# Kernel tuning notes

Hardware: AMD Instinct MI355X
Metric: run time of the kernel (lower is better)

## Reference

```python
import jax, jax.numpy as jnp
import numpy as np

WINDOW = 11
SIGMA = 1.5
CHANNELS = 3
C1 = 0.01 ** 2
C2 = 0.03 ** 2


def _gaussian_kernel(size=WINDOW, sigma=SIGMA, channels=CHANNELS):
    coords = jnp.arange(size, dtype=jnp.float32) - size // 2
    g = jnp.exp(-coords ** 2 / (2.0 * sigma ** 2))
    g = jnp.outer(g, g)
    g = g / g.sum()
    # depthwise kernel: [C, 1, K, K] (OIHW with feature_group_count=C)
    return jnp.broadcast_to(g[None, None], (channels, 1, size, size))


def _dwconv(x, kernel):
    # x: [N, C, H, W]; SAME padding, depthwise (groups = C)
    pad = WINDOW // 2
    return jax.lax.conv_general_dilated(
        x, kernel,
        window_strides=(1, 1),
        padding=[(pad, pad), (pad, pad)],
        dimension_numbers=('NCHW', 'OIHW', 'NCHW'),
        feature_group_count=CHANNELS,
    )


def setup_inputs() -> dict:
    key = jax.random.key(0)
    k1, k2 = jax.random.split(key)
    shape = (16, 3, 512, 512)
    pred = jax.random.uniform(k1, shape, dtype=jnp.float32)
    target = jax.random.uniform(k2, shape, dtype=jnp.float32)
    return {"pred": pred, "target": target}


def reference(pred, target):
    kernel = _gaussian_kernel().astype(pred.dtype)
    mu_p = _dwconv(pred, kernel)
    mu_t = _dwconv(target, kernel)
    mu_p2 = mu_p * mu_p
    mu_t2 = mu_t * mu_t
    mu_pt = mu_p * mu_t
    sigma_p2 = _dwconv(pred * pred, kernel) - mu_p2
    sigma_t2 = _dwconv(target * target, kernel) - mu_t2
    sigma_pt = _dwconv(pred * target, kernel) - mu_pt
    ssim_map = ((2.0 * mu_pt + C1) * (2.0 * sigma_pt + C2)) / (
        (mu_p2 + mu_t2 + C1) * (sigma_p2 + sigma_t2 + C2)
    )
    return 1.0 - ssim_map.mean()
```

## Files before the change

### kernel.cpp

```cpp
#include <hip/hip_runtime.h>
#include <math.h>

#define IMG_H 512
#define IMG_W 512
#define TILE  32
#define NSLOT 64
#define HT_S  52

typedef _Float16 f16x4 __attribute__((ext_vector_type(4)));
typedef _Float16 f16x8 __attribute__((ext_vector_type(8)));
typedef _Float16 h2    __attribute__((ext_vector_type(2)));
typedef float    f32x4 __attribute__((ext_vector_type(4)));

union F16Frag { f16x8 v8; f16x4 v4[2]; };

__global__ __launch_bounds__(256, 8)
void ssim_main(const float* __restrict__ pred, const float* __restrict__ targ,
               float* __restrict__ partial, double* __restrict__ acc, int mode)
{
    __shared__ _Float16 hT[5][TILE][HT_S];

    const int tid  = threadIdx.x;
    const int lane = tid & 63;
    const int wave = tid >> 6;
    const int ln   = lane & 15;
    const int lg   = lane >> 4;

    const int tx = blockIdx.x, ty = blockIdx.y, img = blockIdx.z;
    const float* __restrict__ p = pred + (size_t)img * (IMG_H * IMG_W);
    const float* __restrict__ t = targ + (size_t)img * (IMG_H * IMG_W);
    const int gr0 = ty * TILE - 5;
    const int wo  = tx * TILE - 8;

    if (tid < 160) {
        int q = tid / 32, col = tid & 31;
        *(h2*)&hT[q][col][42] = h2{(_Float16)0.f, (_Float16)0.f};
        *(h2*)&hT[q][col][44] = h2{(_Float16)0.f, (_Float16)0.f};
        *(h2*)&hT[q][col][46] = h2{(_Float16)0.f, (_Float16)0.f};
    }

    f16x8 Bw, A2w;
    #pragma unroll
    for (int j = 0; j < 8; ++j) {
        int k  = lg * 8 + j;
        int ih = k - ln - 3;
        int iv = k - ln;
        float dh = (float)(ih - 5), dv = (float)(iv - 5);
        float vh = 0.26601173f * exp2f(-dh * dh * 0.32059889f);
        float vv = 0.26601173f * exp2f(-dv * dv * 0.32059889f);
        Bw[j]  = (_Float16)(((unsigned)ih <= 10u) ? vh : 0.0f);
        A2w[j] = (_Float16)(((unsigned)iv <= 10u) ? vv : 0.0f);
    }
    const f32x4 zacc = {0.f, 0.f, 0.f, 0.f};

    auto do_tile = [&](int tt) {
        const int rt = tt >> 1, ct = tt & 1;
        const int rowbase = (rt == 2) ? 26 : rt * 16;
        const int gr = gr0 + rowbase + ln;
        const int gc = wo + ct * 16 + lg * 8;
        float4 pv0 = {0,0,0,0}, pv1 = {0,0,0,0}, tv0 = {0,0,0,0}, tv1 = {0,0,0,0};
        if (gr >= 0 && gr < IMG_H && gc >= 0 && gc <= IMG_W - 8) {
            const float* bp = p + (size_t)gr * IMG_W + gc;
            const float* bt = t + (size_t)gr * IMG_W + gc;
            pv0 = ((const float4*)bp)[0]; pv1 = ((const float4*)bp)[1];
            tv0 = ((const float4*)bt)[0]; tv1 = ((const float4*)bt)[1];
        }
        F16Frag pa, ta;
        pa.v8 = f16x8{(_Float16)pv0.x, (_Float16)pv0.y, (_Float16)pv0.z, (_Float16)pv0.w,
                      (_Float16)pv1.x, (_Float16)pv1.y, (_Float16)pv1.z, (_Float16)pv1.w};
        ta.v8 = f16x8{(_Float16)tv0.x, (_Float16)tv0.y, (_Float16)tv0.z, (_Float16)tv0.w,
                      (_Float16)tv1.x, (_Float16)tv1.y, (_Float16)tv1.z, (_Float16)tv1.w};
        f16x8 fq[5];
        fq[0] = pa.v8;
        fq[1] = ta.v8;
        fq[2] = pa.v8 * pa.v8;
        fq[3] = ta.v8 * ta.v8;
        fq[4] = pa.v8 * ta.v8;
        const int ocol = ct * 16 + ln;
        const int orow = rowbase + lg * 4;
        #pragma unroll
        for (int q = 0; q < 5; ++q) {
            f32x4 d = __builtin_amdgcn_mfma_f32_16x16x32_f16(fq[q], Bw, zacc, 0, 0, 0);
            *(h2*)&hT[q][ocol][orow]     = h2{(_Float16)d[0], (_Float16)d[1]};
            *(h2*)&hT[q][ocol][orow + 2] = h2{(_Float16)d[2], (_Float16)d[3]};
        }
    };
    do_tile(wave);
    if (wave < 2) do_tile(wave + 4);
    __syncthreads();

    float lsum = 0.f;
    {
        const int ctv = wave & 1, rtv = wave >> 1;
        const int ocol  = ctv * 16 + ln;
        const int rbase = rtv * 16 + lg * 8;
        f32x4 accq[5];
        #pragma unroll
        for (int q = 0; q < 5; ++q) {
            F16Frag b;
            b.v4[0] = *(const f16x4*)&hT[q][ocol][rbase];
            b.v4[1] = *(const f16x4*)&hT[q][ocol][rbase + 4];
            accq[q] = __builtin_amdgcn_mfma_f32_16x16x32_f16(A2w, b.v8, zacc, 0, 0, 0);
        }
        const float C1 = 1e-4f, C2 = 9e-4f;
        #pragma unroll
        for (int rgi = 0; rgi < 4; ++rgi) {
            float mp = accq[0][rgi], mt = accq[1][rgi];
            float vp = accq[2][rgi] - mp * mp;
            float vt = accq[3][rgi] - mt * mt;
            float cv = accq[4][rgi] - mp * mt;
            float num = (2.f * mp * mt + C1) * (2.f * cv + C2);
            float den = (mp * mp + mt * mt + C1) * (vp + vt + C2);
            lsum = fmaf(num, __builtin_amdgcn_rcpf(den), lsum);
        }
    }

    #pragma unroll
    for (int off = 32; off > 0; off >>= 1)
        lsum += __shfl_down(lsum, off, 64);
    if ((lane) == 0) {
        const int bid = (blockIdx.z * gridDim.y + blockIdx.y) * gridDim.x + blockIdx.x;
        if (mode == 0) {
            partial[bid * 4 + wave] = lsum;
        } else {
            atomicAdd(&acc[(bid * 4 + wave) & (NSLOT - 1)], (double)lsum);
        }
    }
}

__global__ void ssim_init(double* acc)
{
    if (threadIdx.x < NSLOT) acc[threadIdx.x] = 0.0;
}

__global__ __launch_bounds__(256)
void ssim_fin_slots(const float* __restrict__ partial, float* __restrict__ out,
                    int n4, double inv_n)
{
    __shared__ double red[4];
    double s = 0.0;
    const int tid = threadIdx.x;
    for (int i = tid; i < n4; i += 256) {
        float4 v = ((const float4*)partial)[i];
        s += (double)v.x + (double)v.y + (double)v.z + (double)v.w;
    }
    #pragma unroll
    for (int off = 32; off > 0; off >>= 1)
        s += __shfl_down(s, off, 64);
    if ((tid & 63) == 0) red[tid >> 6] = s;
    __syncthreads();
    if (tid == 0)
        out[0] = (float)(1.0 - (red[0] + red[1] + red[2] + red[3]) * inv_n);
}

__global__ void ssim_fin_atomic(const double* __restrict__ acc, float* __restrict__ out,
                                double inv_n)
{
    if (threadIdx.x == 0) {
        double s = 0.0;
        for (int i = 0; i < NSLOT; ++i) s += acc[i];
        out[0] = (float)(1.0 - s * inv_n);
    }
}

extern "C" void kernel_launch(void* const* d_in, const int* in_sizes, int n_in,
                              void* d_out, int out_size, void* d_ws, size_t ws_size,
                              hipStream_t stream)
{
    const float* pred = (const float*)d_in[0];
    const float* targ = (const float*)d_in[1];
    float* out = (float*)d_out;

    const long long total = (long long)in_sizes[0];
    const int n_img = (int)(total / (IMG_H * IMG_W));
    dim3 grid(IMG_W / TILE, IMG_H / TILE, n_img);
    const int nblk = grid.x * grid.y * grid.z;
    const int nslots = nblk * 4;
    const double inv_n = 1.0 / (double)total;

    if (ws_size >= (size_t)nslots * sizeof(float)) {
        float* partial = (float*)d_ws;
        hipLaunchKernelGGL(ssim_main, grid, dim3(256), 0, stream,
                           pred, targ, partial, (double*)nullptr, 0);
        hipLaunchKernelGGL(ssim_fin_slots, dim3(1), dim3(256), 0, stream,
                           partial, out, nslots / 4, inv_n);
    } else {
        double* acc = (double*)d_ws;
        hipLaunchKernelGGL(ssim_init, dim3(1), dim3(64), 0, stream, acc);
        hipLaunchKernelGGL(ssim_main, grid, dim3(256), 0, stream,
                           pred, targ, (float*)nullptr, acc, 1);
        hipLaunchKernelGGL(ssim_fin_atomic, dim3(1), dim3(1), 0, stream,
                           acc, out, inv_n);
    }
}
```

Baseline: 156.4 us.

## Stage input halo tile in shared memory and precompute Gaussian fragments once per block

The main kernel now loads the whole 48x48 input halo region (pred and target, converted to fp16) into shared memory once, with coalesced 8-wide row loads. The MFMA tiles then read from LDS instead of issuing overlapping global loads per wave. The Gaussian weight fragments are computed by 128 threads into shared memory rather than by every lane, and intermediate writes and reads are widened to 8-byte and 16-byte LDS accesses. The final reduction kernel grows to 1024 threads. The cost is more shared memory and an extra barrier, with the occupancy hint lowered from 8 to 5 blocks per CU.

```diff
diff --git a/kernel.cpp b/kernel.cpp
--- a/kernel.cpp
+++ b/kernel.cpp
@@ -5,19 +5,22 @@
 #define IMG_W 512
 #define TILE  32
 #define NSLOT 64
-#define HT_S  52
+#define SAB_R 48
+#define SAB_S 56
+#define HT_S  56
 
 typedef _Float16 f16x4 __attribute__((ext_vector_type(4)));
 typedef _Float16 f16x8 __attribute__((ext_vector_type(8)));
-typedef _Float16 h2    __attribute__((ext_vector_type(2)));
 typedef float    f32x4 __attribute__((ext_vector_type(4)));
 
 union F16Frag { f16x8 v8; f16x4 v4[2]; };
 
-__global__ __launch_bounds__(256, 8)
+__global__ __launch_bounds__(256, 5)
 void ssim_main(const float* __restrict__ pred, const float* __restrict__ targ,
                float* __restrict__ partial, double* __restrict__ acc, int mode)
 {
+    __shared__ _Float16 frags[2][64][8];
+    __shared__ _Float16 sAB[2][SAB_R][SAB_S];
     __shared__ _Float16 hT[5][TILE][HT_S];
 
     const int tid  = threadIdx.x;
@@ -32,44 +35,54 @@
     const int gr0 = ty * TILE - 5;
     const int wo  = tx * TILE - 8;
 
-    if (tid < 160) {
-        int q = tid / 32, col = tid & 31;
-        *(h2*)&hT[q][col][42] = h2{(_Float16)0.f, (_Float16)0.f};
-        *(h2*)&hT[q][col][44] = h2{(_Float16)0.f, (_Float16)0.f};
-        *(h2*)&hT[q][col][46] = h2{(_Float16)0.f, (_Float16)0.f};
-    }
-
-    f16x8 Bw, A2w;
-    #pragma unroll
-    for (int j = 0; j < 8; ++j) {
-        int k  = lg * 8 + j;
-        int ih = k - ln - 3;
-        int iv = k - ln;
-        float dh = (float)(ih - 5), dv = (float)(iv - 5);
-        float vh = 0.26601173f * exp2f(-dh * dh * 0.32059889f);
-        float vv = 0.26601173f * exp2f(-dv * dv * 0.32059889f);
-        Bw[j]  = (_Float16)(((unsigned)ih <= 10u) ? vh : 0.0f);
-        A2w[j] = (_Float16)(((unsigned)iv <= 10u) ? vv : 0.0f);
-    }
+    if (tid < 128) {
+        const int which = tid >> 6, l = tid & 63;
+        const int lln = l & 15, llg = l >> 4;
+        f16x8 f;
+        #pragma unroll
+        for (int j = 0; j < 8; ++j) {
+            int k   = llg * 8 + j;
+            int idx = which ? (k - lln) : (k - lln - 3);
+            float d = (float)(idx - 5);
+            float v = 0.26601173f * exp2f(-d * d * 0.32059889f);
+            f[j] = (_Float16)(((unsigned)idx <= 10u) ? v : 0.0f);
+        }
+        *(f16x8*)&frags[which][l][0] = f;
+    }
+
+    for (int i = tid; i < SAB_R * 6; i += 256) {
+        const int r = i / 6, g = i - 6 * r;
+        const int gr = gr0 + r;
+        const bool in = (gr >= 0) && (gr < IMG_H) &&
+                        !(tx == 0 && g == 0) && !(tx == 15 && g == 5);
+        float4 p0 = {0,0,0,0}, p1 = {0,0,0,0}, t0 = {0,0,0,0}, t1 = {0,0,0,0};
+        if (in) {
+            const float* bp = p + (size_t)gr * IMG_W + (wo + 8 * g);
+            const float* bt = t + (size_t)gr * IMG_W + (wo + 8 * g);
+            p0 = ((const float4*)bp)[0]; p1 = ((const float4*)bp)[1];
+            t0 = ((const float4*)bt)[0]; t1 = ((const float4*)bt)[1];
+        }
+        *(f16x8*)&sAB[0][r][8 * g] =
+            f16x8{(_Float16)p0.x, (_Float16)p0.y, (_Float16)p0.z, (_Float16)p0.w,
+                  (_Float16)p1.x, (_Float16)p1.y, (_Float16)p1.z, (_Float16)p1.w};
+        *(f16x8*)&sAB[1][r][8 * g] =
+            f16x8{(_Float16)t0.x, (_Float16)t0.y, (_Float16)t0.z, (_Float16)t0.w,
+                  (_Float16)t1.x, (_Float16)t1.y, (_Float16)t1.z, (_Float16)t1.w};
+    }
+    __syncthreads();
+
+    const f16x8 Bw  = *(const f16x8*)&frags[0][lane][0];
+    const f16x8 A2w = *(const f16x8*)&frags[1][lane][0];
     const f32x4 zacc = {0.f, 0.f, 0.f, 0.f};
 
     auto do_tile = [&](int tt) {
         const int rt = tt >> 1, ct = tt & 1;
-        const int rowbase = (rt == 2) ? 26 : rt * 16;
-        const int gr = gr0 + rowbase + ln;
-        const int gc = wo + ct * 16 + lg * 8;
-        float4 pv0 = {0,0,0,0}, pv1 = {0,0,0,0}, tv0 = {0,0,0,0}, tv1 = {0,0,0,0};
-        if (gr >= 0 && gr < IMG_H && gc >= 0 && gc <= IMG_W - 8) {
-            const float* bp = p + (size_t)gr * IMG_W + gc;
-            const float* bt = t + (size_t)gr * IMG_W + gc;
-            pv0 = ((const float4*)bp)[0]; pv1 = ((const float4*)bp)[1];
-            tv0 = ((const float4*)bt)[0]; tv1 = ((const float4*)bt)[1];
-        }
+        const int rowbase = rt * 16;
+        const int arow = rowbase + ln;
+        const int acol = ct * 16 + lg * 8;
         F16Frag pa, ta;
-        pa.v8 = f16x8{(_Float16)pv0.x, (_Float16)pv0.y, (_Float16)pv0.z, (_Float16)pv0.w,
-                      (_Float16)pv1.x, (_Float16)pv1.y, (_Float16)pv1.z, (_Float16)pv1.w};
-        ta.v8 = f16x8{(_Float16)tv0.x, (_Float16)tv0.y, (_Float16)tv0.z, (_Float16)tv0.w,
-                      (_Float16)tv1.x, (_Float16)tv1.y, (_Float16)tv1.z, (_Float16)tv1.w};
+        pa.v8 = *(const f16x8*)&sAB[0][arow][acol];
+        ta.v8 = *(const f16x8*)&sAB[1][arow][acol];
         f16x8 fq[5];
         fq[0] = pa.v8;
         fq[1] = ta.v8;
@@ -81,8 +94,8 @@
         #pragma unroll
         for (int q = 0; q < 5; ++q) {
             f32x4 d = __builtin_amdgcn_mfma_f32_16x16x32_f16(fq[q], Bw, zacc, 0, 0, 0);
-            *(h2*)&hT[q][ocol][orow]     = h2{(_Float16)d[0], (_Float16)d[1]};
-            *(h2*)&hT[q][ocol][orow + 2] = h2{(_Float16)d[2], (_Float16)d[3]};
+            *(f16x4*)&hT[q][ocol][orow] =
+                f16x4{(_Float16)d[0], (_Float16)d[1], (_Float16)d[2], (_Float16)d[3]};
         }
     };
     do_tile(wave);
@@ -97,10 +110,8 @@
         f32x4 accq[5];
         #pragma unroll
         for (int q = 0; q < 5; ++q) {
-            F16Frag b;
-            b.v4[0] = *(const f16x4*)&hT[q][ocol][rbase];
-            b.v4[1] = *(const f16x4*)&hT[q][ocol][rbase + 4];
-            accq[q] = __builtin_amdgcn_mfma_f32_16x16x32_f16(A2w, b.v8, zacc, 0, 0, 0);
+            f16x8 b = *(const f16x8*)&hT[q][ocol][rbase];
+            accq[q] = __builtin_amdgcn_mfma_f32_16x16x32_f16(A2w, b, zacc, 0, 0, 0);
         }
         const float C1 = 1e-4f, C2 = 9e-4f;
         #pragma unroll
@@ -118,7 +129,7 @@
     #pragma unroll
     for (int off = 32; off > 0; off >>= 1)
         lsum += __shfl_down(lsum, off, 64);
-    if ((lane) == 0) {
+    if (lane == 0) {
         const int bid = (blockIdx.z * gridDim.y + blockIdx.y) * gridDim.x + blockIdx.x;
         if (mode == 0) {
             partial[bid * 4 + wave] = lsum;
@@ -133,14 +144,14 @@
     if (threadIdx.x < NSLOT) acc[threadIdx.x] = 0.0;
 }
 
-__global__ __launch_bounds__(256)
+__global__ __launch_bounds__(1024)
 void ssim_fin_slots(const float* __restrict__ partial, float* __restrict__ out,
                     int n4, double inv_n)
 {
-    __shared__ double red[4];
+    __shared__ double red[16];
     double s = 0.0;
     const int tid = threadIdx.x;
-    for (int i = tid; i < n4; i += 256) {
+    for (int i = tid; i < n4; i += 1024) {
         float4 v = ((const float4*)partial)[i];
         s += (double)v.x + (double)v.y + (double)v.z + (double)v.w;
     }
@@ -149,8 +160,12 @@
         s += __shfl_down(s, off, 64);
     if ((tid & 63) == 0) red[tid >> 6] = s;
     __syncthreads();
-    if (tid == 0)
-        out[0] = (float)(1.0 - (red[0] + red[1] + red[2] + red[3]) * inv_n);
+    if (tid == 0) {
+        double tot = 0.0;
+        #pragma unroll
+        for (int w = 0; w < 16; ++w) tot += red[w];
+        out[0] = (float)(1.0 - tot * inv_n);
+    }
 }
 
 __global__ void ssim_fin_atomic(const double* __restrict__ acc, float* __restrict__ out,
@@ -182,7 +197,7 @@
         float* partial = (float*)d_ws;
         hipLaunchKernelGGL(ssim_main, grid, dim3(256), 0, stream,
                            pred, targ, partial, (double*)nullptr, 0);
-        hipLaunchKernelGGL(ssim_fin_slots, dim3(1), dim3(256), 0, stream,
+        hipLaunchKernelGGL(ssim_fin_slots, dim3(1), dim3(1024), 0, stream,
                            partial, out, nslots / 4, inv_n);
     } else {
         double* acc = (double*)d_ws;
```

Result: faster. 145.8 us (-6.8%).
